# Kernel tuning notes

Hardware: AMD Instinct MI355X
Metric: run time of the kernel (lower is better)

Reference implementation:

```python
import jax, jax.numpy as jnp
import numpy as np

# dims
B = 4096; BEGIN = 0; END = 2048; N_OBJ = 64; D_OBJ = 32
PI_IN = 31; PI_H = 256; EMB = 256; H = 4; HD = 64; OTH_IN = 256; OTH_H = 256; OTH_OUT = 256

def _lin_init(k, fan_in, fan_out):
    b = np.sqrt(6.0 / (fan_in + fan_out))
    return jax.random.uniform(k, (fan_in, fan_out), jnp.float32, -b, b)

def setup_inputs() -> dict:
    key = jax.random.key(0)
    ks = jax.random.split(key, 8)
    obs = jax.random.normal(ks[0], (B, BEGIN + (END - BEGIN) + OTH_IN), jnp.float32)
    inp = {
        "obs": obs,
        # others encoder MLP: 256 -> 256 -> 256
        "oW1": _lin_init(ks[1], OTH_IN, OTH_H), "ob1": jnp.zeros((OTH_H,), jnp.float32),
        "oW2": _lin_init(ks[2], OTH_H, OTH_OUT), "ob2": jnp.zeros((OTH_OUT,), jnp.float32),
        # per-object pi MLP: 31 -> 256 -> 256 -> 256
        "pW1": _lin_init(ks[3], PI_IN, PI_H), "pb1": jnp.zeros((PI_H,), jnp.float32),
        "pW2": _lin_init(ks[4], PI_H, PI_H), "pb2": jnp.zeros((PI_H,), jnp.float32),
        "pW3": _lin_init(ks[5], PI_H, EMB), "pb3": jnp.zeros((EMB,), jnp.float32),
        # attention projections
        "Wq": _lin_init(ks[6], OTH_OUT, H * HD), "bq": jnp.zeros((H * HD,), jnp.float32),
        # per-head K/V projections (MultiHeadProj): [H, HD, HD], stored as x @ W per head
        "Wk": jax.random.uniform(jax.random.fold_in(key, 10), (H, HD, HD), jnp.float32, -np.sqrt(6.0/(2*HD)), np.sqrt(6.0/(2*HD))),
        "bk": jnp.zeros((H, HD), jnp.float32),
        "Wv": jax.random.uniform(jax.random.fold_in(key, 11), (H, HD, HD), jnp.float32, -np.sqrt(6.0/(2*HD)), np.sqrt(6.0/(2*HD))),
        "bv": jnp.zeros((H, HD), jnp.float32),
    }
    return inp

def reference(obs, oW1, ob1, oW2, ob2, pW1, pb1, pW2, pb2, pW3, pb3, Wq, bq, Wk, bk, Wv, bv):
    # split obs
    objs = obs[:, BEGIN:END].reshape(-1, N_OBJ, D_OBJ)
    others = jnp.concatenate([obs[:, :BEGIN], obs[:, END:]], axis=1)
    # others encoder
    others_e = jax.nn.relu(others @ oW1 + ob1) @ oW2 + ob2           # [B, 256]
    # mask + per-object MLP
    mask = objs[:, :, -1]                                            # [B, N]
    feats = objs[:, :, :-1]                                          # [B, N, 31]
    h = jax.nn.relu(feats @ pW1 + pb1)
    h = jax.nn.relu(h @ pW2 + pb2)
    emb = (h @ pW3 + pb3) * mask[:, :, None]                         # [B, N, EMB]
    # attention
    q = (others_e @ Wq + bq).reshape(-1, H, 1, HD)                   # [B, H, 1, HD]
    e = emb.reshape(-1, N_OBJ, H, HD)                                # [B, N, H, HD]
    key = jnp.einsum('bnhd,hde->bnhe', e, Wk) + bk                   # per-head linear
    val = (jnp.einsum('bnhd,hde->bnhe', e, Wv) + bv) * mask[:, :, None, None]
    logits = jnp.einsum('bhqd,bnhd->bhqn', q, key) / np.sqrt(EMB)    # [B, H, 1, N]
    logits = jnp.where(mask[:, None, None, :] == 0, -1e9, logits)
    attn = jax.nn.softmax(logits, axis=-1)
    out_emb = jnp.einsum('bhqn,bnhd->bhqd', attn, val).reshape(-1, EMB)
    return jnp.concatenate([others_e, out_emb], axis=1)             # [B, 512]
```

## Files before the change

kernel.cpp:

```cpp
#include <hip/hip_runtime.h>

#define BATCH      4096
#define OBS_COLS   2304
#define OTH_OFF    2048
#define EMB        256
#define OUTC       512
#define Q_BYTES    (4096u * 256u * 4u)

typedef __bf16 bf16x8 __attribute__((ext_vector_type(8)));
typedef __bf16 bf16x4 __attribute__((ext_vector_type(4)));
typedef float  f32x16 __attribute__((ext_vector_type(16)));

#define S_PW1  0
#define S_PW2  2
#define S_PW3  18
#define S_OW1  34
#define S_OW2  50
#define S_WQ   66

__device__ __forceinline__ int shx(int row, int col) {
    return (row << 8) + ((((col >> 3) ^ (row & 31)) << 3) | (col & 7));
}

__global__ __launch_bounds__(512) void k_prep(
    const float* __restrict__ pW1, const float* __restrict__ pW2,
    const float* __restrict__ pW3, const float* __restrict__ oW1,
    const float* __restrict__ oW2, const float* __restrict__ Wq,
    __bf16* __restrict__ wp)
{
    const int s = blockIdx.x;
    const int t = threadIdx.x;
    const int ct = t >> 6, lane = t & 63;
    int kt; const float* W; int isW1 = 0;
    if      (s < S_PW2) { kt = s;         W = pW1; isW1 = 1; }
    else if (s < S_PW3) { kt = s - S_PW2; W = pW2; }
    else if (s < S_OW1) { kt = s - S_PW3; W = pW3; }
    else if (s < S_OW2) { kt = s - S_OW1; W = oW1; }
    else if (s < S_WQ)  { kt = s - S_OW2; W = oW2; }
    else                { kt = s - S_WQ;  W = Wq; }
    const int kbase = kt * 16 + (lane >> 5) * 8;
    const int n     = ct * 32 + (lane & 31);
    bf16x8 v;
    #pragma unroll
    for (int j = 0; j < 8; ++j) {
        const int k = kbase + j;
        const float f = (isW1 && k >= 31) ? 0.0f : W[k * 256 + n];
        v[j] = (__bf16)f;
    }
    ((bf16x8*)wp)[(size_t)s * 512 + t] = v;
}

__global__ __launch_bounds__(512, 2) void k_oth(
    const float* __restrict__ obs, const __bf16* __restrict__ wp,
    const float* __restrict__ ob1, const float* __restrict__ ob2,
    const float* __restrict__ bq,
    float* __restrict__ out, float* __restrict__ qg)
{
    __shared__ __align__(16) __bf16 s_a[32 * 256];
    __shared__ __align__(16) __bf16 s_h[32 * 256];

    const int t  = threadIdx.x;
    const int b0 = blockIdx.x * 32;
    const int wv = t >> 6, lane = t & 63;
    const int lm = lane & 31, lh = lane >> 5;
    const int ct = wv;

    #pragma unroll
    for (int i = 0; i < 2; ++i) {
        const int c = i * 512 + t;
        const int row = c >> 5, seg = c & 31;
        const float* src = obs + (size_t)(b0 + row) * OBS_COLS + OTH_OFF + seg * 8;
        const float4 v0 = ((const float4*)src)[0];
        const float4 v1 = ((const float4*)src)[1];
        bf16x8 o;
        o[0]=(__bf16)v0.x; o[1]=(__bf16)v0.y; o[2]=(__bf16)v0.z; o[3]=(__bf16)v0.w;
        o[4]=(__bf16)v1.x; o[5]=(__bf16)v1.y; o[6]=(__bf16)v1.z; o[7]=(__bf16)v1.w;
        *(bf16x8*)&s_a[shx(row, seg * 8)] = o;
    }
    __syncthreads();

    f32x16 acc;
    f32x16 vzero;
    #pragma unroll
    for (int i = 0; i < 16; ++i) vzero[i] = 0.0f;

    {
        const bf16x8* Bg = (const bf16x8*)wp + S_OW1 * 512;
        acc = vzero;
        #pragma unroll
        for (int kt = 0; kt < 16; ++kt) {
            const bf16x8 b = Bg[(kt * 8 + ct) * 64 + lane];
            const bf16x8 a = *(const bf16x8*)&s_a[shx(lm, kt * 16 + lh * 8)];
            acc = __builtin_amdgcn_mfma_f32_32x32x16_bf16(b, a, acc, 0, 0, 0);
        }
        const float* bias = &ob1[ct * 32 + 4 * lh];
        #pragma unroll
        for (int g = 0; g < 4; ++g) {
            bf16x4 v;
            #pragma unroll
            for (int q = 0; q < 4; ++q)
                v[q] = (__bf16)fmaxf(acc[g * 4 + q] + bias[8 * g + q], 0.0f);
            *(bf16x4*)&s_h[(lm << 8) + ((((ct << 2) + g) ^ lm) << 3) + 4 * lh] = v;
        }
    }
    __syncthreads();

    {
        const bf16x8* Bg = (const bf16x8*)wp + S_OW2 * 512;
        acc = vzero;
        #pragma unroll
        for (int kt = 0; kt < 16; ++kt) {
            const bf16x8 b = Bg[(kt * 8 + ct) * 64 + lane];
            const bf16x8 a = *(const bf16x8*)&s_h[shx(lm, kt * 16 + lh * 8)];
            acc = __builtin_amdgcn_mfma_f32_32x32x16_bf16(b, a, acc, 0, 0, 0);
        }
        const float* bias = &ob2[ct * 32 + 4 * lh];
        float* dstg = &out[(size_t)(b0 + lm) * OUTC + ct * 32 + 4 * lh];
        #pragma unroll
        for (int g = 0; g < 4; ++g) {
            float4 fv; bf16x4 v;
            float* fp = &fv.x;
            #pragma unroll
            for (int q = 0; q < 4; ++q) {
                const float f = acc[g * 4 + q] + bias[8 * g + q];
                fp[q] = f; v[q] = (__bf16)f;
            }
            *(float4*)&dstg[8 * g] = fv;
            *(bf16x4*)&s_a[(lm << 8) + ((((ct << 2) + g) ^ lm) << 3) + 4 * lh] = v;
        }
    }
    __syncthreads();

    {
        const bf16x8* Bg = (const bf16x8*)wp + S_WQ * 512;
        acc = vzero;
        #pragma unroll
        for (int kt = 0; kt < 16; ++kt) {
            const bf16x8 b = Bg[(kt * 8 + ct) * 64 + lane];
            const bf16x8 a = *(const bf16x8*)&s_a[shx(lm, kt * 16 + lh * 8)];
            acc = __builtin_amdgcn_mfma_f32_32x32x16_bf16(b, a, acc, 0, 0, 0);
        }
        const float* bias = &bq[ct * 32 + 4 * lh];
        float* dstg = &qg[(size_t)(b0 + lm) * 256 + ct * 32 + 4 * lh];
        #pragma unroll
        for (int g = 0; g < 4; ++g) {
            float4 fv;
            float* fp = &fv.x;
            #pragma unroll
            for (int q = 0; q < 4; ++q)
                fp[q] = acc[g * 4 + q] + bias[8 * g + q];
            *(float4*)&dstg[8 * g] = fv;
        }
    }
}

__global__ __launch_bounds__(512, 4) void k_obj(
    const float* __restrict__ obs,  const __bf16* __restrict__ wp,
    const float* __restrict__ pb1,  const float* __restrict__ pb2,
    const float* __restrict__ pb3,  const float* __restrict__ qg,
    const float* __restrict__ bk,   const float* __restrict__ Wk,
    const float* __restrict__ bv,   const float* __restrict__ Wv,
    float* __restrict__ out)
{
    __shared__ __align__(16) __bf16 s_h[128 * 256];
    __shared__ __align__(16) char s_fp[128 * 40 * 2];
    __bf16* s_f = (__bf16*)s_fp;
    float*  s_p = (float*)s_fp;
    __shared__ float s_mask[128];
    __shared__ float s_qk[8 * 64];
    __shared__ float s_am[8 * 64];
    __shared__ float s_amsum[8];

    const int t  = threadIdx.x;
    const int b0 = blockIdx.x * 2;
    const int wv = t >> 6, lane = t & 63;
    const int lm = lane & 31, lh = lane >> 5;
    const int rtp = wv & 1;
    const int ct0 = (wv >> 1) * 2;
    const int row0 = rtp * 64 + lm;
    const int row1 = row0 + 32;

    {
        const int row = t >> 2, q4 = t & 3;
        const float* src = obs + (size_t)(b0 + (row >> 6)) * OBS_COLS
                               + (row & 63) * 32 + q4 * 8;
        const float4 v0 = ((const float4*)src)[0];
        const float4 v1 = ((const float4*)src)[1];
        bf16x8 o;
        o[0]=(__bf16)v0.x; o[1]=(__bf16)v0.y; o[2]=(__bf16)v0.z; o[3]=(__bf16)v0.w;
        o[4]=(__bf16)v1.x; o[5]=(__bf16)v1.y; o[6]=(__bf16)v1.z; o[7]=(__bf16)v1.w;
        *(bf16x8*)&s_f[row * 40 + q4 * 8] = o;
        if (q4 == 3) s_mask[row] = v1.w;
    }
    __syncthreads();

    f32x16 acc[2][2];
    f32x16 vzero;
    #pragma unroll
    for (int i = 0; i < 16; ++i) vzero[i] = 0.0f;

    {
        const bf16x8* Bg = (const bf16x8*)wp + S_PW1 * 512;
        #pragma unroll
        for (int r = 0; r < 2; ++r)
            #pragma unroll
            for (int c = 0; c < 2; ++c) acc[r][c] = vzero;
        #pragma unroll
        for (int kt = 0; kt < 2; ++kt) {
            const bf16x8 bf0 = Bg[(kt * 8 + ct0 + 0) * 64 + lane];
            const bf16x8 bf1 = Bg[(kt * 8 + ct0 + 1) * 64 + lane];
            const bf16x8 a0 = *(const bf16x8*)&s_f[row0 * 40 + kt * 16 + lh * 8];
            const bf16x8 a1 = *(const bf16x8*)&s_f[row1 * 40 + kt * 16 + lh * 8];
            acc[0][0] = __builtin_amdgcn_mfma_f32_32x32x16_bf16(bf0, a0, acc[0][0], 0, 0, 0);
            acc[0][1] = __builtin_amdgcn_mfma_f32_32x32x16_bf16(bf1, a0, acc[0][1], 0, 0, 0);
            acc[1][0] = __builtin_amdgcn_mfma_f32_32x32x16_bf16(bf0, a1, acc[1][0], 0, 0, 0);
            acc[1][1] = __builtin_amdgcn_mfma_f32_32x32x16_bf16(bf1, a1, acc[1][1], 0, 0, 0);
        }
        #pragma unroll
        for (int r = 0; r < 2; ++r) {
            const int row = r ? row1 : row0;
            #pragma unroll
            for (int c = 0; c < 2; ++c) {
                const float* bias = &pb1[(ct0 + c) * 32 + 4 * lh];
                #pragma unroll
                for (int g = 0; g < 4; ++g) {
                    bf16x4 v;
                    #pragma unroll
                    for (int q = 0; q < 4; ++q)
                        v[q] = (__bf16)fmaxf(acc[r][c][g * 4 + q] + bias[8 * g + q], 0.0f);
                    *(bf16x4*)&s_h[(row << 8) + (((((ct0 + c) << 2) + g) ^ lm) << 3) + 4 * lh] = v;
                }
            }
        }
    }
    __syncthreads();

    {
        const bf16x8* Bg = (const bf16x8*)wp + S_PW2 * 512;
        #pragma unroll
        for (int r = 0; r < 2; ++r)
            #pragma unroll
            for (int c = 0; c < 2; ++c) acc[r][c] = vzero;
        bf16x8 bc0 = Bg[(ct0 + 0) * 64 + lane];
        bf16x8 bc1 = Bg[(ct0 + 1) * 64 + lane];
        #pragma unroll 4
        for (int kt = 0; kt < 16; ++kt) {
            const int kn = (kt + 1) & 15;
            const bf16x8 bn0 = Bg[(kn * 8 + ct0 + 0) * 64 + lane];
            const bf16x8 bn1 = Bg[(kn * 8 + ct0 + 1) * 64 + lane];
            const bf16x8 a0 = *(const bf16x8*)&s_h[(row0 << 8) + (((2 * kt + lh) ^ lm) << 3)];
            const bf16x8 a1 = *(const bf16x8*)&s_h[(row1 << 8) + (((2 * kt + lh) ^ lm) << 3)];
            acc[0][0] = __builtin_amdgcn_mfma_f32_32x32x16_bf16(bc0, a0, acc[0][0], 0, 0, 0);
            acc[0][1] = __builtin_amdgcn_mfma_f32_32x32x16_bf16(bc1, a0, acc[0][1], 0, 0, 0);
            acc[1][0] = __builtin_amdgcn_mfma_f32_32x32x16_bf16(bc0, a1, acc[1][0], 0, 0, 0);
            acc[1][1] = __builtin_amdgcn_mfma_f32_32x32x16_bf16(bc1, a1, acc[1][1], 0, 0, 0);
            bc0 = bn0; bc1 = bn1;
        }
        __syncthreads();
        #pragma unroll
        for (int r = 0; r < 2; ++r) {
            const int row = r ? row1 : row0;
            #pragma unroll
            for (int c = 0; c < 2; ++c) {
                const float* bias = &pb2[(ct0 + c) * 32 + 4 * lh];
                #pragma unroll
                for (int g = 0; g < 4; ++g) {
                    bf16x4 v;
                    #pragma unroll
                    for (int q = 0; q < 4; ++q)
                        v[q] = (__bf16)fmaxf(acc[r][c][g * 4 + q] + bias[8 * g + q], 0.0f);
                    *(bf16x4*)&s_h[(row << 8) + (((((ct0 + c) << 2) + g) ^ lm) << 3) + 4 * lh] = v;
                }
            }
        }
    }
    __syncthreads();

    {
        const bf16x8* Bg = (const bf16x8*)wp + S_PW3 * 512;
        #pragma unroll
        for (int r = 0; r < 2; ++r)
            #pragma unroll
            for (int c = 0; c < 2; ++c) acc[r][c] = vzero;
        bf16x8 bc0 = Bg[(ct0 + 0) * 64 + lane];
        bf16x8 bc1 = Bg[(ct0 + 1) * 64 + lane];
        #pragma unroll 4
        for (int kt = 0; kt < 16; ++kt) {
            const int kn = (kt + 1) & 15;
            const bf16x8 bn0 = Bg[(kn * 8 + ct0 + 0) * 64 + lane];
            const bf16x8 bn1 = Bg[(kn * 8 + ct0 + 1) * 64 + lane];
            const bf16x8 a0 = *(const bf16x8*)&s_h[(row0 << 8) + (((2 * kt + lh) ^ lm) << 3)];
            const bf16x8 a1 = *(const bf16x8*)&s_h[(row1 << 8) + (((2 * kt + lh) ^ lm) << 3)];
            acc[0][0] = __builtin_amdgcn_mfma_f32_32x32x16_bf16(bc0, a0, acc[0][0], 0, 0, 0);
            acc[0][1] = __builtin_amdgcn_mfma_f32_32x32x16_bf16(bc1, a0, acc[0][1], 0, 0, 0);
            acc[1][0] = __builtin_amdgcn_mfma_f32_32x32x16_bf16(bc0, a1, acc[1][0], 0, 0, 0);
            acc[1][1] = __builtin_amdgcn_mfma_f32_32x32x16_bf16(bc1, a1, acc[1][1], 0, 0, 0);
            bc0 = bn0; bc1 = bn1;
        }
        __syncthreads();
        #pragma unroll
        for (int r = 0; r < 2; ++r) {
            const int row = r ? row1 : row0;
            const float mk = s_mask[row];
            #pragma unroll
            for (int c = 0; c < 2; ++c) {
                const float* bias = &pb3[(ct0 + c) * 32 + 4 * lh];
                #pragma unroll
                for (int g = 0; g < 4; ++g) {
                    bf16x4 v;
                    #pragma unroll
                    for (int q = 0; q < 4; ++q)
                        v[q] = (__bf16)((acc[r][c][g * 4 + q] + bias[8 * g + q]) * mk);
                    *(bf16x4*)&s_h[(row << 8) + (((((ct0 + c) << 2) + g) ^ lm) << 3) + 4 * lh] = v;
                }
            }
        }
    }
    __syncthreads();

    {
        const int r = t >> 8, h = (t >> 6) & 3, d = t & 63;
        const float* wkr = Wk + ((size_t)h * 64 + d) * 64;
        const float* q_r = qg + (size_t)(b0 + r) * 256 + h * 64;
        float a = 0.0f;
        for (int e = 0; e < 64; e += 4) {
            const float4 w = *(const float4*)&wkr[e];
            const float4 q = *(const float4*)&q_r[e];
            a += w.x * q.x + w.y * q.y + w.z * q.z + w.w * q.w;
        }
        s_qk[(r * 4 + h) * 64 + d] = a;
    }
    __syncthreads();

    {
        const int r = wv >> 2, h = wv & 3;
        const float* q_r = qg + (size_t)(b0 + r) * 256 + h * 64;
        float qb = q_r[lane] * bk[h * 64 + lane];
        #pragma unroll
        for (int off = 32; off > 0; off >>= 1) qb += __shfl_xor(qb, off, 64);
        const int erow = r * 64 + lane;
        float dot = 0.0f;
        #pragma unroll
        for (int d8 = 0; d8 < 8; ++d8) {
            const bf16x8 ev = *(const bf16x8*)&s_h[(erow << 8) + ((((h << 3) + d8) ^ (erow & 31)) << 3)];
            const float* kv = &s_qk[(r * 4 + h) * 64 + d8 * 8];
            #pragma unroll
            for (int j = 0; j < 8; ++j) dot += (float)ev[j] * kv[j];
        }
        const float mk = s_mask[erow];
        float logit = (dot + qb) * 0.0625f;
        if (mk == 0.0f) logit = -1.0e9f;
        float m = logit;
        #pragma unroll
        for (int off = 32; off > 0; off >>= 1) m = fmaxf(m, __shfl_xor(m, off, 64));
        const float ex = __expf(logit - m);
        float ssum = ex;
        #pragma unroll
        for (int off = 32; off > 0; off >>= 1) ssum += __shfl_xor(ssum, off, 64);
        const float am = (ex / ssum) * mk;
        s_am[(r * 4 + h) * 64 + lane] = am;
        float ams = am;
        #pragma unroll
        for (int off = 32; off > 0; off >>= 1) ams += __shfl_xor(ams, off, 64);
        if (lane == 0) s_amsum[r * 4 + h] = ams;
    }
    __syncthreads();

    {
        const int r = t >> 8, h = (t >> 6) & 3, d = t & 63;
        const float* amr = &s_am[(r * 4 + h) * 64];
        const int blkbase = (h << 3) + (d >> 3);
        const int doff = d & 7;
        float a = 0.0f;
        for (int n = 0; n < 64; ++n) {
            const int row = r * 64 + n;
            a += amr[n] * (float)s_h[(row << 8) + (((blkbase ^ (row & 31)) << 3) | doff)];
        }
        s_p[(r * 4 + h) * 64 + d] = a;
    }
    __syncthreads();

    {
        const int r = t >> 8, h = (t >> 6) & 3, e = t & 63;
        float a = s_amsum[r * 4 + h] * bv[h * 64 + e];
        const float* pr  = &s_p[(r * 4 + h) * 64];
        const float* wvp = Wv + (size_t)h * 64 * 64;
        for (int d = 0; d < 64; ++d)
            a += pr[d] * wvp[d * 64 + e];
        out[(size_t)(b0 + r) * OUTC + EMB + h * 64 + e] = a;
    }
}

extern "C" void kernel_launch(void* const* d_in, const int* in_sizes, int n_in,
                              void* d_out, int out_size, void* d_ws, size_t ws_size,
                              hipStream_t stream)
{
    const float* obs = (const float*)d_in[0];
    const float* oW1 = (const float*)d_in[1];
    const float* ob1 = (const float*)d_in[2];
    const float* oW2 = (const float*)d_in[3];
    const float* ob2 = (const float*)d_in[4];
    const float* pW1 = (const float*)d_in[5];
    const float* pb1 = (const float*)d_in[6];
    const float* pW2 = (const float*)d_in[7];
    const float* pb2 = (const float*)d_in[8];
    const float* pW3 = (const float*)d_in[9];
    const float* pb3 = (const float*)d_in[10];
    const float* Wq  = (const float*)d_in[11];
    const float* bq  = (const float*)d_in[12];
    const float* Wk  = (const float*)d_in[13];
    const float* bk  = (const float*)d_in[14];
    const float* Wv  = (const float*)d_in[15];
    const float* bv  = (const float*)d_in[16];
    float*  out = (float*)d_out;
    float*  qg  = (float*)d_ws;
    __bf16* wp  = (__bf16*)((char*)d_ws + Q_BYTES);

    k_prep<<<82, 512, 0, stream>>>(pW1, pW2, pW3, oW1, oW2, Wq, wp);
    k_oth<<<BATCH / 32, 512, 0, stream>>>(obs, wp, ob1, ob2, bq, out, qg);
    k_obj<<<BATCH / 2, 512, 0, stream>>>(obs, wp, pb1, pb2, pb3, qg,
                                         bk, Wk, bv, Wv, out);
}
```

Baseline: 264.7 us.

## Fold weight prep into others kernel and precompute q·Wk per row

Removes the separate prep kernel: the others-encoder blocks now read fp32 oW1/oW2/Wq directly and convert them to bf16 in registers, while the first 34 blocks also pack the pi-MLP weights. The others kernel additionally computes q·Wk with MFMA and the q·bk bias term per head, storing them to workspace. This removes the per-batch qk matvec stage and one barrier from the object kernel. The object kernel also preloads its first-layer weights before the obs load and unrolls the attention and Wv loops. One launch is saved, at the cost of redundant fp32 weight reads and conversions in every others block.

```diff
diff --git a/kernel.cpp b/kernel.cpp
--- a/kernel.cpp
+++ b/kernel.cpp
@@ -5,7 +5,9 @@
 #define OTH_OFF    2048
 #define EMB        256
 #define OUTC       512
-#define Q_BYTES    (4096u * 256u * 4u)
+
+#define QK_BYTES   (4096u * 256u * 4u)
+#define QB_BYTES   (4096u * 4u * 4u)
 
 typedef __bf16 bf16x8 __attribute__((ext_vector_type(8)));
 typedef __bf16 bf16x4 __attribute__((ext_vector_type(4)));
@@ -14,56 +16,51 @@
 #define S_PW1  0
 #define S_PW2  2
 #define S_PW3  18
-#define S_OW1  34
-#define S_OW2  50
-#define S_WQ   66
+#define N_SLICE 34
 
 __device__ __forceinline__ int shx(int row, int col) {
     return (row << 8) + ((((col >> 3) ^ (row & 31)) << 3) | (col & 7));
 }
 
-__global__ __launch_bounds__(512) void k_prep(
+__global__ __launch_bounds__(512, 2) void k_oth(
+    const float* __restrict__ obs,
+    const float* __restrict__ oW1, const float* __restrict__ ob1,
+    const float* __restrict__ oW2, const float* __restrict__ ob2,
+    const float* __restrict__ Wq,  const float* __restrict__ bq,
+    const float* __restrict__ Wk,  const float* __restrict__ bk,
     const float* __restrict__ pW1, const float* __restrict__ pW2,
-    const float* __restrict__ pW3, const float* __restrict__ oW1,
-    const float* __restrict__ oW2, const float* __restrict__ Wq,
-    __bf16* __restrict__ wp)
-{
-    const int s = blockIdx.x;
-    const int t = threadIdx.x;
-    const int ct = t >> 6, lane = t & 63;
-    int kt; const float* W; int isW1 = 0;
-    if      (s < S_PW2) { kt = s;         W = pW1; isW1 = 1; }
-    else if (s < S_PW3) { kt = s - S_PW2; W = pW2; }
-    else if (s < S_OW1) { kt = s - S_PW3; W = pW3; }
-    else if (s < S_OW2) { kt = s - S_OW1; W = oW1; }
-    else if (s < S_WQ)  { kt = s - S_OW2; W = oW2; }
-    else                { kt = s - S_WQ;  W = Wq; }
-    const int kbase = kt * 16 + (lane >> 5) * 8;
-    const int n     = ct * 32 + (lane & 31);
-    bf16x8 v;
-    #pragma unroll
-    for (int j = 0; j < 8; ++j) {
-        const int k = kbase + j;
-        const float f = (isW1 && k >= 31) ? 0.0f : W[k * 256 + n];
-        v[j] = (__bf16)f;
-    }
-    ((bf16x8*)wp)[(size_t)s * 512 + t] = v;
-}
-
-__global__ __launch_bounds__(512, 2) void k_oth(
-    const float* __restrict__ obs, const __bf16* __restrict__ wp,
-    const float* __restrict__ ob1, const float* __restrict__ ob2,
-    const float* __restrict__ bq,
-    float* __restrict__ out, float* __restrict__ qg)
+    const float* __restrict__ pW3,
+    float* __restrict__ out, float* __restrict__ qkg,
+    float* __restrict__ qbg, __bf16* __restrict__ wp)
 {
     __shared__ __align__(16) __bf16 s_a[32 * 256];
     __shared__ __align__(16) __bf16 s_h[32 * 256];
+    __shared__ __align__(16) __bf16 s_q[32 * 256];
+    __shared__ float s_qb[32 * 4];
 
     const int t  = threadIdx.x;
     const int b0 = blockIdx.x * 32;
     const int wv = t >> 6, lane = t & 63;
     const int lm = lane & 31, lh = lane >> 5;
     const int ct = wv;
+
+    if (blockIdx.x < N_SLICE) {
+        const int s = blockIdx.x;
+        int kt; const float* W; int isW1 = 0;
+        if      (s < S_PW2) { kt = s;         W = pW1; isW1 = 1; }
+        else if (s < S_PW3) { kt = s - S_PW2; W = pW2; }
+        else                { kt = s - S_PW3; W = pW3; }
+        const int kbase = kt * 16 + lh * 8;
+        const int n     = (t >> 6) * 32 + lm;
+        bf16x8 v;
+        #pragma unroll
+        for (int j = 0; j < 8; ++j) {
+            const int k = kbase + j;
+            const float f = (isW1 && k >= 31) ? 0.0f : W[k * 256 + n];
+            v[j] = (__bf16)f;
+        }
+        ((bf16x8*)wp)[(size_t)s * 512 + t] = v;
+    }
 
     #pragma unroll
     for (int i = 0; i < 2; ++i) {
@@ -77,6 +74,7 @@
         o[4]=(__bf16)v1.x; o[5]=(__bf16)v1.y; o[6]=(__bf16)v1.z; o[7]=(__bf16)v1.w;
         *(bf16x8*)&s_a[shx(row, seg * 8)] = o;
     }
+    if (t < 128) s_qb[t] = 0.0f;
     __syncthreads();
 
     f32x16 acc;
@@ -85,13 +83,24 @@
     for (int i = 0; i < 16; ++i) vzero[i] = 0.0f;
 
     {
-        const bf16x8* Bg = (const bf16x8*)wp + S_OW1 * 512;
+        const float* Wl = oW1 + (size_t)(lh * 8) * 256 + ct * 32 + lm;
         acc = vzero;
-        #pragma unroll
+        float f[8];
+        #pragma unroll
+        for (int j = 0; j < 8; ++j) f[j] = Wl[j * 256];
+        #pragma unroll 4
         for (int kt = 0; kt < 16; ++kt) {
-            const bf16x8 b = Bg[(kt * 8 + ct) * 64 + lane];
+            float fn[8];
+            const int kn = (kt + 1) & 15;
+            #pragma unroll
+            for (int j = 0; j < 8; ++j) fn[j] = Wl[(kn * 16 + j) * 256];
+            bf16x8 b;
+            #pragma unroll
+            for (int j = 0; j < 8; ++j) b[j] = (__bf16)f[j];
             const bf16x8 a = *(const bf16x8*)&s_a[shx(lm, kt * 16 + lh * 8)];
             acc = __builtin_amdgcn_mfma_f32_32x32x16_bf16(b, a, acc, 0, 0, 0);
+            #pragma unroll
+            for (int j = 0; j < 8; ++j) f[j] = fn[j];
         }
         const float* bias = &ob1[ct * 32 + 4 * lh];
         #pragma unroll
@@ -106,13 +115,24 @@
     __syncthreads();
 
     {
-        const bf16x8* Bg = (const bf16x8*)wp + S_OW2 * 512;
+        const float* Wl = oW2 + (size_t)(lh * 8) * 256 + ct * 32 + lm;
         acc = vzero;
-        #pragma unroll
+        float f[8];
+        #pragma unroll
+        for (int j = 0; j < 8; ++j) f[j] = Wl[j * 256];
+        #pragma unroll 4
         for (int kt = 0; kt < 16; ++kt) {
-            const bf16x8 b = Bg[(kt * 8 + ct) * 64 + lane];
+            float fn[8];
+            const int kn = (kt + 1) & 15;
+            #pragma unroll
+            for (int j = 0; j < 8; ++j) fn[j] = Wl[(kn * 16 + j) * 256];
+            bf16x8 b;
+            #pragma unroll
+            for (int j = 0; j < 8; ++j) b[j] = (__bf16)f[j];
             const bf16x8 a = *(const bf16x8*)&s_h[shx(lm, kt * 16 + lh * 8)];
             acc = __builtin_amdgcn_mfma_f32_32x32x16_bf16(b, a, acc, 0, 0, 0);
+            #pragma unroll
+            for (int j = 0; j < 8; ++j) f[j] = fn[j];
         }
         const float* bias = &ob2[ct * 32 + 4 * lh];
         float* dstg = &out[(size_t)(b0 + lm) * OUTC + ct * 32 + 4 * lh];
@@ -122,8 +142,8 @@
             float* fp = &fv.x;
             #pragma unroll
             for (int q = 0; q < 4; ++q) {
-                const float f = acc[g * 4 + q] + bias[8 * g + q];
-                fp[q] = f; v[q] = (__bf16)f;
+                const float f2 = acc[g * 4 + q] + bias[8 * g + q];
+                fp[q] = f2; v[q] = (__bf16)f2;
             }
             *(float4*)&dstg[8 * g] = fv;
             *(bf16x4*)&s_a[(lm << 8) + ((((ct << 2) + g) ^ lm) << 3) + 4 * lh] = v;
@@ -132,23 +152,68 @@
     __syncthreads();
 
     {
-        const bf16x8* Bg = (const bf16x8*)wp + S_WQ * 512;
+        const float* Wl = Wq + (size_t)(lh * 8) * 256 + ct * 32 + lm;
         acc = vzero;
-        #pragma unroll
+        float f[8];
+        #pragma unroll
+        for (int j = 0; j < 8; ++j) f[j] = Wl[j * 256];
+        #pragma unroll 4
         for (int kt = 0; kt < 16; ++kt) {
-            const bf16x8 b = Bg[(kt * 8 + ct) * 64 + lane];
+            float fn[8];
+            const int kn = (kt + 1) & 15;
+            #pragma unroll
+            for (int j = 0; j < 8; ++j) fn[j] = Wl[(kn * 16 + j) * 256];
+            bf16x8 b;
+            #pragma unroll
+            for (int j = 0; j < 8; ++j) b[j] = (__bf16)f[j];
             const bf16x8 a = *(const bf16x8*)&s_a[shx(lm, kt * 16 + lh * 8)];
             acc = __builtin_amdgcn_mfma_f32_32x32x16_bf16(b, a, acc, 0, 0, 0);
-        }
+            #pragma unroll
+            for (int j = 0; j < 8; ++j) f[j] = fn[j];
+        }
+        const int hh = ct >> 1;
         const float* bias = &bq[ct * 32 + 4 * lh];
-        float* dstg = &qg[(size_t)(b0 + lm) * 256 + ct * 32 + 4 * lh];
+        const float* bkp  = &bk[ct * 32 + 4 * lh];
+        float part = 0.0f;
+        #pragma unroll
+        for (int g = 0; g < 4; ++g) {
+            bf16x4 v;
+            #pragma unroll
+            for (int q = 0; q < 4; ++q) {
+                const float f2 = acc[g * 4 + q] + bias[8 * g + q];
+                part += f2 * bkp[8 * g + q];
+                v[q] = (__bf16)f2;
+            }
+            *(bf16x4*)&s_q[(lm << 8) + ((((ct << 2) + g) ^ lm) << 3) + 4 * lh] = v;
+        }
+        part += __shfl_xor(part, 32, 64);
+        if (lane < 32) atomicAdd(&s_qb[lm * 4 + hh], part);
+    }
+    __syncthreads();
+
+    if (t < 128) qbg[(size_t)(b0 + (t >> 2)) * 4 + (t & 3)] = s_qb[t];
+
+    {
+        const int h = wv >> 1, c2 = wv & 1;
+        acc = vzero;
+        #pragma unroll
+        for (int kt = 0; kt < 4; ++kt) {
+            const float* wk = Wk + ((size_t)(h * 64 + c2 * 32 + lm) * 64 + kt * 16 + lh * 8);
+            const float4 w0 = *(const float4*)wk;
+            const float4 w1 = *(const float4*)(wk + 4);
+            bf16x8 b;
+            b[0]=(__bf16)w0.x; b[1]=(__bf16)w0.y; b[2]=(__bf16)w0.z; b[3]=(__bf16)w0.w;
+            b[4]=(__bf16)w1.x; b[5]=(__bf16)w1.y; b[6]=(__bf16)w1.z; b[7]=(__bf16)w1.w;
+            const bf16x8 a = *(const bf16x8*)&s_q[shx(lm, h * 64 + kt * 16 + lh * 8)];
+            acc = __builtin_amdgcn_mfma_f32_32x32x16_bf16(b, a, acc, 0, 0, 0);
+        }
+        float* dstg = &qkg[(size_t)(b0 + lm) * 256 + h * 64 + c2 * 32 + 4 * lh];
         #pragma unroll
         for (int g = 0; g < 4; ++g) {
             float4 fv;
             float* fp = &fv.x;
             #pragma unroll
-            for (int q = 0; q < 4; ++q)
-                fp[q] = acc[g * 4 + q] + bias[8 * g + q];
+            for (int q = 0; q < 4; ++q) fp[q] = acc[g * 4 + q];
             *(float4*)&dstg[8 * g] = fv;
         }
     }
@@ -157,10 +222,9 @@
 __global__ __launch_bounds__(512, 4) void k_obj(
     const float* __restrict__ obs,  const __bf16* __restrict__ wp,
     const float* __restrict__ pb1,  const float* __restrict__ pb2,
-    const float* __restrict__ pb3,  const float* __restrict__ qg,
-    const float* __restrict__ bk,   const float* __restrict__ Wk,
-    const float* __restrict__ bv,   const float* __restrict__ Wv,
-    float* __restrict__ out)
+    const float* __restrict__ pb3,  const float* __restrict__ qkg,
+    const float* __restrict__ qbg,  const float* __restrict__ bv,
+    const float* __restrict__ Wv,   float* __restrict__ out)
 {
     __shared__ __align__(16) __bf16 s_h[128 * 256];
     __shared__ __align__(16) char s_fp[128 * 40 * 2];
@@ -179,6 +243,16 @@
     const int ct0 = (wv >> 1) * 2;
     const int row0 = rtp * 64 + lm;
     const int row1 = row0 + 32;
+
+    bf16x8 b1[2][2];
+    {
+        const bf16x8* Bg = (const bf16x8*)wp + S_PW1 * 512;
+        #pragma unroll
+        for (int kt = 0; kt < 2; ++kt)
+            #pragma unroll
+            for (int c = 0; c < 2; ++c)
+                b1[kt][c] = Bg[(kt * 8 + ct0 + c) * 64 + lane];
+    }
 
     {
         const int row = t >> 2, q4 = t & 3;
@@ -192,6 +266,7 @@
         *(bf16x8*)&s_f[row * 40 + q4 * 8] = o;
         if (q4 == 3) s_mask[row] = v1.w;
     }
+    if (t < 128) ((float4*)s_qk)[t] = ((const float4*)(qkg + (size_t)b0 * 256))[t];
     __syncthreads();
 
     f32x16 acc[2][2];
@@ -200,21 +275,18 @@
     for (int i = 0; i < 16; ++i) vzero[i] = 0.0f;
 
     {
-        const bf16x8* Bg = (const bf16x8*)wp + S_PW1 * 512;
         #pragma unroll
         for (int r = 0; r < 2; ++r)
             #pragma unroll
             for (int c = 0; c < 2; ++c) acc[r][c] = vzero;
         #pragma unroll
         for (int kt = 0; kt < 2; ++kt) {
-            const bf16x8 bf0 = Bg[(kt * 8 + ct0 + 0) * 64 + lane];
-            const bf16x8 bf1 = Bg[(kt * 8 + ct0 + 1) * 64 + lane];
             const bf16x8 a0 = *(const bf16x8*)&s_f[row0 * 40 + kt * 16 + lh * 8];
             const bf16x8 a1 = *(const bf16x8*)&s_f[row1 * 40 + kt * 16 + lh * 8];
-            acc[0][0] = __builtin_amdgcn_mfma_f32_32x32x16_bf16(bf0, a0, acc[0][0], 0, 0, 0);
-            acc[0][1] = __builtin_amdgcn_mfma_f32_32x32x16_bf16(bf1, a0, acc[0][1], 0, 0, 0);
-            acc[1][0] = __builtin_amdgcn_mfma_f32_32x32x16_bf16(bf0, a1, acc[1][0], 0, 0, 0);
-            acc[1][1] = __builtin_amdgcn_mfma_f32_32x32x16_bf16(bf1, a1, acc[1][1], 0, 0, 0);
+            acc[0][0] = __builtin_amdgcn_mfma_f32_32x32x16_bf16(b1[kt][0], a0, acc[0][0], 0, 0, 0);
+            acc[0][1] = __builtin_amdgcn_mfma_f32_32x32x16_bf16(b1[kt][1], a0, acc[0][1], 0, 0, 0);
+            acc[1][0] = __builtin_amdgcn_mfma_f32_32x32x16_bf16(b1[kt][0], a1, acc[1][0], 0, 0, 0);
+            acc[1][1] = __builtin_amdgcn_mfma_f32_32x32x16_bf16(b1[kt][1], a1, acc[1][1], 0, 0, 0);
         }
         #pragma unroll
         for (int r = 0; r < 2; ++r) {
@@ -319,25 +391,8 @@
     __syncthreads();
 
     {
-        const int r = t >> 8, h = (t >> 6) & 3, d = t & 63;
-        const float* wkr = Wk + ((size_t)h * 64 + d) * 64;
-        const float* q_r = qg + (size_t)(b0 + r) * 256 + h * 64;
-        float a = 0.0f;
-        for (int e = 0; e < 64; e += 4) {
-            const float4 w = *(const float4*)&wkr[e];
-            const float4 q = *(const float4*)&q_r[e];
-            a += w.x * q.x + w.y * q.y + w.z * q.z + w.w * q.w;
-        }
-        s_qk[(r * 4 + h) * 64 + d] = a;
-    }
-    __syncthreads();
-
-    {
         const int r = wv >> 2, h = wv & 3;
-        const float* q_r = qg + (size_t)(b0 + r) * 256 + h * 64;
-        float qb = q_r[lane] * bk[h * 64 + lane];
-        #pragma unroll
-        for (int off = 32; off > 0; off >>= 1) qb += __shfl_xor(qb, off, 64);
+        const float qb = qbg[(size_t)(b0 + r) * 4 + h];
         const int erow = r * 64 + lane;
         float dot = 0.0f;
         #pragma unroll
@@ -372,6 +427,7 @@
         const int blkbase = (h << 3) + (d >> 3);
         const int doff = d & 7;
         float a = 0.0f;
+        #pragma unroll 16
         for (int n = 0; n < 64; ++n) {
             const int row = r * 64 + n;
             a += amr[n] * (float)s_h[(row << 8) + (((blkbase ^ (row & 31)) << 3) | doff)];
@@ -384,9 +440,10 @@
         const int r = t >> 8, h = (t >> 6) & 3, e = t & 63;
         float a = s_amsum[r * 4 + h] * bv[h * 64 + e];
         const float* pr  = &s_p[(r * 4 + h) * 64];
-        const float* wvp = Wv + (size_t)h * 64 * 64;
+        const float* wvp = Wv + (size_t)h * 64 * 64 + e;
+        #pragma unroll 16
         for (int d = 0; d < 64; ++d)
-            a += pr[d] * wvp[d * 64 + e];
+            a += pr[d] * wvp[d * 64];
         out[(size_t)(b0 + r) * OUTC + EMB + h * 64 + e] = a;
     }
 }
@@ -413,11 +470,13 @@
     const float* Wv  = (const float*)d_in[15];
     const float* bv  = (const float*)d_in[16];
     float*  out = (float*)d_out;
-    float*  qg  = (float*)d_ws;
-    __bf16* wp  = (__bf16*)((char*)d_ws + Q_BYTES);
-
-    k_prep<<<82, 512, 0, stream>>>(pW1, pW2, pW3, oW1, oW2, Wq, wp);
-    k_oth<<<BATCH / 32, 512, 0, stream>>>(obs, wp, ob1, ob2, bq, out, qg);
-    k_obj<<<BATCH / 2, 512, 0, stream>>>(obs, wp, pb1, pb2, pb3, qg,
-                                         bk, Wk, bv, Wv, out);
+    float*  qkg = (float*)d_ws;
+    float*  qbg = (float*)((char*)d_ws + QK_BYTES);
+    __bf16* wp  = (__bf16*)((char*)d_ws + QK_BYTES + QB_BYTES);
+
+    k_oth<<<BATCH / 32, 512, 0, stream>>>(obs, oW1, ob1, oW2, ob2, Wq, bq,
+                                          Wk, bk, pW1, pW2, pW3,
+                                          out, qkg, qbg, wp);
+    k_obj<<<BATCH / 2, 512, 0, stream>>>(obs, wp, pb1, pb2, pb3, qkg, qbg,
+                                         bv, Wv, out);
 }
```

Result: faster. 229.6 us (-13.3%).

## Fuse others-encoder into object kernel and fold Wq·Wk into prepacked weights

Applied to the files above, without the earlier changes.

Removes the separate k_oth launch. Each k_obj block now runs the others MLP and the query projection for its own 2 batch rows, padded to a 32-row MFMA tile, so the qg workspace round trip goes away. Wq is algebraically combined with the per-head Wk, and the bias cross-terms are folded in k_prep, so the query·key vector comes straight out of one GEMM. This drops the per-block Wk loop. Smaller changes: pW1 fragments are prefetched into registers, the next weight fragments are loaded ahead of each MFMA, and the attention loops get unroll pragmas. The cost is that every block repeats the 256x256 GEMMs on a mostly-zero 32-row tile, which is much more total MFMA work.

```diff
diff --git a/kernel.cpp b/kernel.cpp
--- a/kernel.cpp
+++ b/kernel.cpp
@@ -5,7 +5,8 @@
 #define OTH_OFF    2048
 #define EMB        256
 #define OUTC       512
-#define Q_BYTES    (4096u * 256u * 4u)
+
+#define FOLD_BYTES 8192u
 
 typedef __bf16 bf16x8 __attribute__((ext_vector_type(8)));
 typedef __bf16 bf16x4 __attribute__((ext_vector_type(4)));
@@ -16,7 +17,7 @@
 #define S_PW3  18
 #define S_OW1  34
 #define S_OW2  50
-#define S_WQ   66
+#define S_WQK  66
 
 __device__ __forceinline__ int shx(int row, int col) {
     return (row << 8) + ((((col >> 3) ^ (row & 31)) << 3) | (col & 7));
@@ -26,141 +27,82 @@
     const float* __restrict__ pW1, const float* __restrict__ pW2,
     const float* __restrict__ pW3, const float* __restrict__ oW1,
     const float* __restrict__ oW2, const float* __restrict__ Wq,
-    __bf16* __restrict__ wp)
+    const float* __restrict__ Wk,  const float* __restrict__ bq,
+    const float* __restrict__ bk,
+    float* __restrict__ fold, __bf16* __restrict__ wp)
 {
     const int s = blockIdx.x;
     const int t = threadIdx.x;
-    const int ct = t >> 6, lane = t & 63;
-    int kt; const float* W; int isW1 = 0;
-    if      (s < S_PW2) { kt = s;         W = pW1; isW1 = 1; }
-    else if (s < S_PW3) { kt = s - S_PW2; W = pW2; }
-    else if (s < S_OW1) { kt = s - S_PW3; W = pW3; }
-    else if (s < S_OW2) { kt = s - S_OW1; W = oW1; }
-    else if (s < S_WQ)  { kt = s - S_OW2; W = oW2; }
-    else                { kt = s - S_WQ;  W = Wq; }
-    const int kbase = kt * 16 + (lane >> 5) * 8;
-    const int n     = ct * 32 + (lane & 31);
-    bf16x8 v;
-    #pragma unroll
-    for (int j = 0; j < 8; ++j) {
-        const int k = kbase + j;
-        const float f = (isW1 && k >= 31) ? 0.0f : W[k * 256 + n];
-        v[j] = (__bf16)f;
-    }
-    ((bf16x8*)wp)[(size_t)s * 512 + t] = v;
-}
-
-__global__ __launch_bounds__(512, 2) void k_oth(
-    const float* __restrict__ obs, const __bf16* __restrict__ wp,
-    const float* __restrict__ ob1, const float* __restrict__ ob2,
-    const float* __restrict__ bq,
-    float* __restrict__ out, float* __restrict__ qg)
-{
-    __shared__ __align__(16) __bf16 s_a[32 * 256];
-    __shared__ __align__(16) __bf16 s_h[32 * 256];
-
-    const int t  = threadIdx.x;
-    const int b0 = blockIdx.x * 32;
-    const int wv = t >> 6, lane = t & 63;
-    const int lm = lane & 31, lh = lane >> 5;
-    const int ct = wv;
-
-    #pragma unroll
-    for (int i = 0; i < 2; ++i) {
-        const int c = i * 512 + t;
-        const int row = c >> 5, seg = c & 31;
-        const float* src = obs + (size_t)(b0 + row) * OBS_COLS + OTH_OFF + seg * 8;
-        const float4 v0 = ((const float4*)src)[0];
-        const float4 v1 = ((const float4*)src)[1];
-        bf16x8 o;
-        o[0]=(__bf16)v0.x; o[1]=(__bf16)v0.y; o[2]=(__bf16)v0.z; o[3]=(__bf16)v0.w;
-        o[4]=(__bf16)v1.x; o[5]=(__bf16)v1.y; o[6]=(__bf16)v1.z; o[7]=(__bf16)v1.w;
-        *(bf16x8*)&s_a[shx(row, seg * 8)] = o;
-    }
-    __syncthreads();
-
-    f32x16 acc;
-    f32x16 vzero;
-    #pragma unroll
-    for (int i = 0; i < 16; ++i) vzero[i] = 0.0f;
-
-    {
-        const bf16x8* Bg = (const bf16x8*)wp + S_OW1 * 512;
-        acc = vzero;
-        #pragma unroll
-        for (int kt = 0; kt < 16; ++kt) {
-            const bf16x8 b = Bg[(kt * 8 + ct) * 64 + lane];
-            const bf16x8 a = *(const bf16x8*)&s_a[shx(lm, kt * 16 + lh * 8)];
-            acc = __builtin_amdgcn_mfma_f32_32x32x16_bf16(b, a, acc, 0, 0, 0);
-        }
-        const float* bias = &ob1[ct * 32 + 4 * lh];
-        #pragma unroll
-        for (int g = 0; g < 4; ++g) {
-            bf16x4 v;
-            #pragma unroll
-            for (int q = 0; q < 4; ++q)
-                v[q] = (__bf16)fmaxf(acc[g * 4 + q] + bias[8 * g + q], 0.0f);
-            *(bf16x4*)&s_h[(lm << 8) + ((((ct << 2) + g) ^ lm) << 3) + 4 * lh] = v;
-        }
-    }
-    __syncthreads();
-
-    {
-        const bf16x8* Bg = (const bf16x8*)wp + S_OW2 * 512;
-        acc = vzero;
-        #pragma unroll
-        for (int kt = 0; kt < 16; ++kt) {
-            const bf16x8 b = Bg[(kt * 8 + ct) * 64 + lane];
-            const bf16x8 a = *(const bf16x8*)&s_h[shx(lm, kt * 16 + lh * 8)];
-            acc = __builtin_amdgcn_mfma_f32_32x32x16_bf16(b, a, acc, 0, 0, 0);
-        }
-        const float* bias = &ob2[ct * 32 + 4 * lh];
-        float* dstg = &out[(size_t)(b0 + lm) * OUTC + ct * 32 + 4 * lh];
-        #pragma unroll
-        for (int g = 0; g < 4; ++g) {
-            float4 fv; bf16x4 v;
-            float* fp = &fv.x;
-            #pragma unroll
-            for (int q = 0; q < 4; ++q) {
-                const float f = acc[g * 4 + q] + bias[8 * g + q];
-                fp[q] = f; v[q] = (__bf16)f;
-            }
-            *(float4*)&dstg[8 * g] = fv;
-            *(bf16x4*)&s_a[(lm << 8) + ((((ct << 2) + g) ^ lm) << 3) + 4 * lh] = v;
-        }
-    }
-    __syncthreads();
-
-    {
-        const bf16x8* Bg = (const bf16x8*)wp + S_WQ * 512;
-        acc = vzero;
-        #pragma unroll
-        for (int kt = 0; kt < 16; ++kt) {
-            const bf16x8 b = Bg[(kt * 8 + ct) * 64 + lane];
-            const bf16x8 a = *(const bf16x8*)&s_a[shx(lm, kt * 16 + lh * 8)];
-            acc = __builtin_amdgcn_mfma_f32_32x32x16_bf16(b, a, acc, 0, 0, 0);
-        }
-        const float* bias = &bq[ct * 32 + 4 * lh];
-        float* dstg = &qg[(size_t)(b0 + lm) * 256 + ct * 32 + 4 * lh];
-        #pragma unroll
-        for (int g = 0; g < 4; ++g) {
-            float4 fv;
-            float* fp = &fv.x;
-            #pragma unroll
-            for (int q = 0; q < 4; ++q)
-                fp[q] = acc[g * 4 + q] + bias[8 * g + q];
-            *(float4*)&dstg[8 * g] = fv;
+    if (s < 82) {
+        const int ct = t >> 6, lane = t & 63;
+        const int n  = ct * 32 + (lane & 31);
+        bf16x8 v;
+        if (s < S_WQK) {
+            int kt; const float* W; int isW1 = 0;
+            if      (s < S_PW2) { kt = s;         W = pW1; isW1 = 1; }
+            else if (s < S_PW3) { kt = s - S_PW2; W = pW2; }
+            else if (s < S_OW1) { kt = s - S_PW3; W = pW3; }
+            else if (s < S_OW2) { kt = s - S_OW1; W = oW1; }
+            else                { kt = s - S_OW2; W = oW2; }
+            const int kbase = kt * 16 + (lane >> 5) * 8;
+            #pragma unroll
+            for (int j = 0; j < 8; ++j) {
+                const int k = kbase + j;
+                const float f = (isW1 && k >= 31) ? 0.0f : W[k * 256 + n];
+                v[j] = (__bf16)f;
+            }
+        } else {
+            const int kt = s - S_WQK;
+            const int kbase = kt * 16 + (lane >> 5) * 8;
+            const int h = n >> 6, d = n & 63;
+            const int qb_ = n & ~63;
+            const float* wk = Wk + (size_t)h * 4096 + (size_t)d * 64;
+            float acc[8];
+            #pragma unroll
+            for (int j = 0; j < 8; ++j) acc[j] = 0.0f;
+            for (int e = 0; e < 64; ++e) {
+                const float wkv = wk[e];
+                #pragma unroll
+                for (int j = 0; j < 8; ++j)
+                    acc[j] += Wq[(size_t)(kbase + j) * 256 + qb_ + e] * wkv;
+            }
+            #pragma unroll
+            for (int j = 0; j < 8; ++j) v[j] = (__bf16)acc[j];
+        }
+        ((bf16x8*)wp)[(size_t)s * 512 + t] = v;
+    } else {
+        if (t < 256) {
+            const int h = t >> 6, d = t & 63;
+            const float* wk = Wk + (size_t)h * 4096 + (size_t)d * 64;
+            const float* bqs = bq + (t & ~63);
+            float a = 0.0f;
+            for (int e = 0; e < 64; ++e) a += wk[e] * bqs[e];
+            fold[t] = a;
+        }
+        #pragma unroll
+        for (int i = 0; i < 2; ++i) {
+            const int idx = i * 512 + t;
+            const int c = idx >> 2, h = idx & 3;
+            float a = 0.0f;
+            for (int e = 0; e < 64; ++e)
+                a += Wq[(size_t)c * 256 + h * 64 + e] * bk[h * 64 + e];
+            fold[256 + idx] = a;
+        }
+        if (t < 4) {
+            float a = 0.0f;
+            for (int e = 0; e < 64; ++e) a += bq[t * 64 + e] * bk[t * 64 + e];
+            fold[1280 + t] = a;
         }
     }
 }
 
 __global__ __launch_bounds__(512, 4) void k_obj(
     const float* __restrict__ obs,  const __bf16* __restrict__ wp,
+    const float* __restrict__ fold,
+    const float* __restrict__ ob1,  const float* __restrict__ ob2,
     const float* __restrict__ pb1,  const float* __restrict__ pb2,
-    const float* __restrict__ pb3,  const float* __restrict__ qg,
-    const float* __restrict__ bk,   const float* __restrict__ Wk,
-    const float* __restrict__ bv,   const float* __restrict__ Wv,
-    float* __restrict__ out)
+    const float* __restrict__ pb3,  const float* __restrict__ bv,
+    const float* __restrict__ Wv,   float* __restrict__ out)
 {
     __shared__ __align__(16) __bf16 s_h[128 * 256];
     __shared__ __align__(16) char s_fp[128 * 40 * 2];
@@ -170,6 +112,7 @@
     __shared__ float s_qk[8 * 64];
     __shared__ float s_am[8 * 64];
     __shared__ float s_amsum[8];
+    __shared__ float s_qb[8];
 
     const int t  = threadIdx.x;
     const int b0 = blockIdx.x * 2;
@@ -179,6 +122,17 @@
     const int ct0 = (wv >> 1) * 2;
     const int row0 = rtp * 64 + lm;
     const int row1 = row0 + 32;
+    const int ct = wv;
+
+    bf16x8 b1[2][2];
+    {
+        const bf16x8* Bg = (const bf16x8*)wp + S_PW1 * 512;
+        #pragma unroll
+        for (int kt = 0; kt < 2; ++kt)
+            #pragma unroll
+            for (int c = 0; c < 2; ++c)
+                b1[kt][c] = Bg[(kt * 8 + ct0 + c) * 64 + lane];
+    }
 
     {
         const int row = t >> 2, q4 = t & 3;
@@ -192,6 +146,29 @@
         *(bf16x8*)&s_f[row * 40 + q4 * 8] = o;
         if (q4 == 3) s_mask[row] = v1.w;
     }
+    if (t < 64) {
+        const int r = t >> 5, seg = t & 31;
+        const float* src = obs + (size_t)(b0 + r) * OBS_COLS + OTH_OFF + seg * 8;
+        const float4 v0 = ((const float4*)src)[0];
+        const float4 v1 = ((const float4*)src)[1];
+        bf16x8 o;
+        o[0]=(__bf16)v0.x; o[1]=(__bf16)v0.y; o[2]=(__bf16)v0.z; o[3]=(__bf16)v0.w;
+        o[4]=(__bf16)v1.x; o[5]=(__bf16)v1.y; o[6]=(__bf16)v1.z; o[7]=(__bf16)v1.w;
+        *(bf16x8*)&s_h[shx(96 + r, seg * 8)] = o;
+    }
+    {
+        bf16x8 z;
+        #pragma unroll
+        for (int j = 0; j < 8; ++j) z[j] = (__bf16)0.0f;
+        #pragma unroll
+        for (int i = 0; i < 2; ++i) {
+            const int u = i * 512 + t;
+            if (u < 960) {
+                const int row = 98 + (u >> 5), seg = u & 31;
+                *(bf16x8*)&s_h[shx(row, seg * 8)] = z;
+            }
+        }
+    }
     __syncthreads();
 
     f32x16 acc[2][2];
@@ -200,21 +177,110 @@
     for (int i = 0; i < 16; ++i) vzero[i] = 0.0f;
 
     {
-        const bf16x8* Bg = (const bf16x8*)wp + S_PW1 * 512;
+        const bf16x8* Bg = (const bf16x8*)wp + S_OW1 * 512;
+        f32x16 a1 = vzero;
+        bf16x8 bc = Bg[ct * 64 + lane];
+        bf16x8 bn = Bg[(8 + ct) * 64 + lane];
+        #pragma unroll 4
+        for (int kt = 0; kt < 16; ++kt) {
+            const bf16x8 b2 = Bg[((((kt + 2) & 15)) * 8 + ct) * 64 + lane];
+            const bf16x8 a = *(const bf16x8*)&s_h[shx(96 + lm, kt * 16 + lh * 8)];
+            a1 = __builtin_amdgcn_mfma_f32_32x32x16_bf16(bc, a, a1, 0, 0, 0);
+            bc = bn; bn = b2;
+        }
+        const float* bias = &ob1[ct * 32 + 4 * lh];
+        #pragma unroll
+        for (int g = 0; g < 4; ++g) {
+            bf16x4 v;
+            #pragma unroll
+            for (int q = 0; q < 4; ++q)
+                v[q] = (__bf16)fmaxf(a1[g * 4 + q] + bias[8 * g + q], 0.0f);
+            *(bf16x4*)&s_h[((64 + lm) << 8) + ((((ct << 2) + g) ^ lm) << 3) + 4 * lh] = v;
+        }
+    }
+    __syncthreads();
+
+    {
+        const bf16x8* Bg = (const bf16x8*)wp + S_OW2 * 512;
+        f32x16 a1 = vzero;
+        bf16x8 bc = Bg[ct * 64 + lane];
+        bf16x8 bn = Bg[(8 + ct) * 64 + lane];
+        #pragma unroll 4
+        for (int kt = 0; kt < 16; ++kt) {
+            const bf16x8 b2 = Bg[((((kt + 2) & 15)) * 8 + ct) * 64 + lane];
+            const bf16x8 a = *(const bf16x8*)&s_h[shx(64 + lm, kt * 16 + lh * 8)];
+            a1 = __builtin_amdgcn_mfma_f32_32x32x16_bf16(bc, a, a1, 0, 0, 0);
+            bc = bn; bn = b2;
+        }
+        const float* bias = &ob2[ct * 32 + 4 * lh];
+        #pragma unroll
+        for (int g = 0; g < 4; ++g) {
+            float4 fv; bf16x4 v;
+            float* fp = &fv.x;
+            #pragma unroll
+            for (int q = 0; q < 4; ++q) {
+                const float f2 = a1[g * 4 + q] + bias[8 * g + q];
+                fp[q] = f2; v[q] = (__bf16)f2;
+            }
+            if (lm < 2)
+                *(float4*)&out[(size_t)(b0 + lm) * OUTC + ct * 32 + 4 * lh + 8 * g] = fv;
+            *(bf16x4*)&s_h[((96 + lm) << 8) + ((((ct << 2) + g) ^ lm) << 3) + 4 * lh] = v;
+        }
+    }
+    __syncthreads();
+
+    {
+        const bf16x8* Bg = (const bf16x8*)wp + S_WQK * 512;
+        f32x16 a1 = vzero;
+        bf16x8 bc = Bg[ct * 64 + lane];
+        bf16x8 bn = Bg[(8 + ct) * 64 + lane];
+        #pragma unroll 4
+        for (int kt = 0; kt < 16; ++kt) {
+            const bf16x8 b2 = Bg[((((kt + 2) & 15)) * 8 + ct) * 64 + lane];
+            const bf16x8 a = *(const bf16x8*)&s_h[shx(96 + lm, kt * 16 + lh * 8)];
+            a1 = __builtin_amdgcn_mfma_f32_32x32x16_bf16(bc, a, a1, 0, 0, 0);
+            bc = bn; bn = b2;
+        }
+        if (lm < 2) {
+            const int h = ct >> 1;
+            #pragma unroll
+            for (int g = 0; g < 4; ++g)
+                #pragma unroll
+                for (int q = 0; q < 4; ++q) {
+                    const int n = ct * 32 + 4 * lh + 8 * g + q;
+                    const int d = (ct & 1) * 32 + 4 * lh + 8 * g + q;
+                    s_qk[(lm * 4 + h) * 64 + d] = a1[g * 4 + q] + fold[n];
+                }
+        }
+        {
+            const int r = wv >> 2, h = wv & 3;
+            float pq = 0.0f;
+            #pragma unroll
+            for (int i = 0; i < 4; ++i) {
+                const int c = lane + i * 64;
+                const float ec = (float)s_h[shx(96 + r, c)];
+                pq += ec * fold[256 + c * 4 + h];
+            }
+            #pragma unroll
+            for (int off = 32; off > 0; off >>= 1) pq += __shfl_xor(pq, off, 64);
+            if (lane == 0) s_qb[wv] = pq + fold[1280 + h];
+        }
+    }
+    __syncthreads();
+
+    {
         #pragma unroll
         for (int r = 0; r < 2; ++r)
             #pragma unroll
             for (int c = 0; c < 2; ++c) acc[r][c] = vzero;
         #pragma unroll
         for (int kt = 0; kt < 2; ++kt) {
-            const bf16x8 bf0 = Bg[(kt * 8 + ct0 + 0) * 64 + lane];
-            const bf16x8 bf1 = Bg[(kt * 8 + ct0 + 1) * 64 + lane];
             const bf16x8 a0 = *(const bf16x8*)&s_f[row0 * 40 + kt * 16 + lh * 8];
             const bf16x8 a1 = *(const bf16x8*)&s_f[row1 * 40 + kt * 16 + lh * 8];
-            acc[0][0] = __builtin_amdgcn_mfma_f32_32x32x16_bf16(bf0, a0, acc[0][0], 0, 0, 0);
-            acc[0][1] = __builtin_amdgcn_mfma_f32_32x32x16_bf16(bf1, a0, acc[0][1], 0, 0, 0);
-            acc[1][0] = __builtin_amdgcn_mfma_f32_32x32x16_bf16(bf0, a1, acc[1][0], 0, 0, 0);
-            acc[1][1] = __builtin_amdgcn_mfma_f32_32x32x16_bf16(bf1, a1, acc[1][1], 0, 0, 0);
+            acc[0][0] = __builtin_amdgcn_mfma_f32_32x32x16_bf16(b1[kt][0], a0, acc[0][0], 0, 0, 0);
+            acc[0][1] = __builtin_amdgcn_mfma_f32_32x32x16_bf16(b1[kt][1], a0, acc[0][1], 0, 0, 0);
+            acc[1][0] = __builtin_amdgcn_mfma_f32_32x32x16_bf16(b1[kt][0], a1, acc[1][0], 0, 0, 0);
+            acc[1][1] = __builtin_amdgcn_mfma_f32_32x32x16_bf16(b1[kt][1], a1, acc[1][1], 0, 0, 0);
         }
         #pragma unroll
         for (int r = 0; r < 2; ++r) {
@@ -319,25 +385,8 @@
     __syncthreads();
 
     {
-        const int r = t >> 8, h = (t >> 6) & 3, d = t & 63;
-        const float* wkr = Wk + ((size_t)h * 64 + d) * 64;
-        const float* q_r = qg + (size_t)(b0 + r) * 256 + h * 64;
-        float a = 0.0f;
-        for (int e = 0; e < 64; e += 4) {
-            const float4 w = *(const float4*)&wkr[e];
-            const float4 q = *(const float4*)&q_r[e];
-            a += w.x * q.x + w.y * q.y + w.z * q.z + w.w * q.w;
-        }
-        s_qk[(r * 4 + h) * 64 + d] = a;
-    }
-    __syncthreads();
-
-    {
         const int r = wv >> 2, h = wv & 3;
-        const float* q_r = qg + (size_t)(b0 + r) * 256 + h * 64;
-        float qb = q_r[lane] * bk[h * 64 + lane];
-        #pragma unroll
-        for (int off = 32; off > 0; off >>= 1) qb += __shfl_xor(qb, off, 64);
+        const float qb = s_qb[wv];
         const int erow = r * 64 + lane;
         float dot = 0.0f;
         #pragma unroll
@@ -372,6 +421,7 @@
         const int blkbase = (h << 3) + (d >> 3);
         const int doff = d & 7;
         float a = 0.0f;
+        #pragma unroll 16
         for (int n = 0; n < 64; ++n) {
             const int row = r * 64 + n;
             a += amr[n] * (float)s_h[(row << 8) + (((blkbase ^ (row & 31)) << 3) | doff)];
@@ -384,9 +434,10 @@
         const int r = t >> 8, h = (t >> 6) & 3, e = t & 63;
         float a = s_amsum[r * 4 + h] * bv[h * 64 + e];
         const float* pr  = &s_p[(r * 4 + h) * 64];
-        const float* wvp = Wv + (size_t)h * 64 * 64;
+        const float* wvp = Wv + (size_t)h * 64 * 64 + e;
+        #pragma unroll 16
         for (int d = 0; d < 64; ++d)
-            a += pr[d] * wvp[d * 64 + e];
+            a += pr[d] * wvp[d * 64];
         out[(size_t)(b0 + r) * OUTC + EMB + h * 64 + e] = a;
     }
 }
@@ -412,12 +463,12 @@
     const float* bk  = (const float*)d_in[14];
     const float* Wv  = (const float*)d_in[15];
     const float* bv  = (const float*)d_in[16];
-    float*  out = (float*)d_out;
-    float*  qg  = (float*)d_ws;
-    __bf16* wp  = (__bf16*)((char*)d_ws + Q_BYTES);
-
-    k_prep<<<82, 512, 0, stream>>>(pW1, pW2, pW3, oW1, oW2, Wq, wp);
-    k_oth<<<BATCH / 32, 512, 0, stream>>>(obs, wp, ob1, ob2, bq, out, qg);
-    k_obj<<<BATCH / 2, 512, 0, stream>>>(obs, wp, pb1, pb2, pb3, qg,
-                                         bk, Wk, bv, Wv, out);
+    float*  out  = (float*)d_out;
+    float*  fold = (float*)d_ws;
+    __bf16* wp   = (__bf16*)((char*)d_ws + FOLD_BYTES);
+
+    k_prep<<<83, 512, 0, stream>>>(pW1, pW2, pW3, oW1, oW2, Wq, Wk, bq, bk,
+                                   fold, wp);
+    k_obj<<<BATCH / 2, 512, 0, stream>>>(obs, wp, fold, ob1, ob2,
+                                         pb1, pb2, pb3, bv, Wv, out);
 }
```

New measurement: 270.4 us. 1.02x slower.
